# Optimization experiments

Measured on AMD Instinct MI355X. Metric: run time of the kernel, lower is better.

The kernel has to match this reference:

```python
import jax, jax.numpy as jnp
import numpy as np

B, S, D, H, DK, DV, DFF, L, V = 8, 1024, 256, 8, 32, 32, 1024, 4, 28
EPS = 1e-5
NEG = -1e9


def _ln(x, w, b):
    m = jnp.mean(x, axis=-1, keepdims=True)
    v = jnp.var(x, axis=-1, keepdims=True)
    return (x - m) * jax.lax.rsqrt(v + EPS) * w + b


def setup_inputs() -> dict:
    key = jax.random.key(0)
    ks = jax.random.split(key, 30)
    std = 0.02
    inp = {
        'input_ids': jax.random.randint(ks[0], (B, S), 0, V),
        'tok_embed': jax.random.normal(ks[1], (V, D), jnp.float32) * std,
        'pos_embed': jax.random.normal(ks[2], (S, D), jnp.float32) * std,
        'emb_ln_w': jnp.ones((D,), jnp.float32),
        'emb_ln_b': jnp.zeros((D,), jnp.float32),
        'Wq': jax.random.normal(ks[3], (L, D, H * DK), jnp.float32) * std,
        'bq': jnp.zeros((L, H * DK), jnp.float32),
        'Wk': jax.random.normal(ks[4], (L, D, H * DK), jnp.float32) * std,
        'bk': jnp.zeros((L, H * DK), jnp.float32),
        'Wv': jax.random.normal(ks[5], (L, D, H * DV), jnp.float32) * std,
        'bv': jnp.zeros((L, H * DV), jnp.float32),
        'Wo': jax.random.normal(ks[6], (L, H * DV, D), jnp.float32) * std,
        'bo': jnp.zeros((L, D), jnp.float32),
        'ln_w': jnp.ones((L, D), jnp.float32),
        'ln_b': jnp.zeros((L, D), jnp.float32),
        'W1': jax.random.normal(ks[7], (L, D, DFF), jnp.float32) * std,
        'b1': jnp.zeros((L, DFF), jnp.float32),
        'W2': jax.random.normal(ks[8], (L, DFF, D), jnp.float32) * std,
        'b2': jnp.zeros((L, D), jnp.float32),
        'ft1_w': jax.random.normal(ks[9], (D, D), jnp.float32) * std,
        'ft1_b': jnp.zeros((D,), jnp.float32),
        'ft2_w': jax.random.normal(ks[10], (D, D // 2), jnp.float32) * std,
        'ft2_b': jnp.zeros((D // 2,), jnp.float32),
        'cls_w': jax.random.normal(ks[11], (D // 2, 2), jnp.float32) * std,
        'cls_b': jnp.zeros((2,), jnp.float32),
    }
    return inp


def reference(input_ids, tok_embed, pos_embed, emb_ln_w, emb_ln_b,
              Wq, bq, Wk, bk, Wv, bv, Wo, bo, ln_w, ln_b,
              W1, b1, W2, b2, ft1_w, ft1_b, ft2_w, ft2_b, cls_w, cls_b):
    # Embedding: tok + pos, then LayerNorm
    x = tok_embed[input_ids] + pos_embed[jnp.arange(S)][None, :, :]
    x = _ln(x, emb_ln_w, emb_ln_b)
    # pad mask: True where key position is pad (token id 0); broadcast [B,1,1,S]
    pad = (input_ids == 0)[:, None, None, :]
    scale = 1.0 / np.sqrt(DK)
    for i in range(L):
        residual = x
        q = (x @ Wq[i] + bq[i]).reshape(B, S, H, DK).transpose(0, 2, 1, 3)
        k = (x @ Wk[i] + bk[i]).reshape(B, S, H, DK).transpose(0, 2, 1, 3)
        v = (x @ Wv[i] + bv[i]).reshape(B, S, H, DV).transpose(0, 2, 1, 3)
        scores = jnp.einsum('bhqd,bhkd->bhqk', q, k) * scale
        scores = jnp.where(pad, NEG, scores)
        attn = jax.nn.softmax(scores, axis=-1)
        ctx = jnp.einsum('bhqk,bhkd->bhqd', attn, v)
        ctx = ctx.transpose(0, 2, 1, 3).reshape(B, S, H * DV)
        x = _ln(ctx @ Wo[i] + bo[i] + residual, ln_w[i], ln_b[i])
        # FFN (note: original has NO residual/norm after FFN)
        x = jax.nn.relu(x @ W1[i] + b1[i]) @ W2[i] + b2[i]
    cls = x[:, 0, :]
    feat = jax.nn.relu(cls @ ft1_w + ft1_b) @ ft2_w + ft2_b  # dropout = eval no-op
    logits = feat @ cls_w + cls_b
    return logits, feat
```

## Files before the change

kernel.cpp:

```cpp
#include <hip/hip_runtime.h>
#include <math.h>

#define S_ 1024
#define D_ 256

typedef __attribute__((ext_vector_type(8))) _Float16 half8;
typedef __attribute__((ext_vector_type(4))) _Float16 half4;
typedef __attribute__((ext_vector_type(2))) _Float16 half2v;
typedef __attribute__((ext_vector_type(4))) float f32x4;
typedef __attribute__((ext_vector_type(4))) unsigned int u32x4;

__device__ __forceinline__ float wave_sum64(float x) {
    x += __shfl_xor(x, 32); x += __shfl_xor(x, 16); x += __shfl_xor(x, 8);
    x += __shfl_xor(x, 4);  x += __shfl_xor(x, 2);  x += __shfl_xor(x, 1);
    return x;
}

#define GLD16(gp, lp) __builtin_amdgcn_global_load_lds( \
    (const __attribute__((address_space(1))) void*)(gp), \
    (__attribute__((address_space(3))) void*)(lp), 16, 0, 0)

__global__ __launch_bounds__(256) void transpose_cvt(
    const float* __restrict__ src, _Float16* __restrict__ dst, int K, int N)
{
    __shared__ float tile[32][33];
    src += (size_t)blockIdx.z * K * N;
    dst += (size_t)blockIdx.z * K * N;
    const int bx = blockIdx.x * 32;
    const int by = blockIdx.y * 32;
    const int t = threadIdx.x;
    const int c = t & 31, r0 = t >> 5;
    #pragma unroll
    for (int j = 0; j < 4; ++j)
        tile[r0 + 8 * j][c] = src[(size_t)(by + r0 + 8 * j) * N + bx + c];
    __syncthreads();
    #pragma unroll
    for (int j = 0; j < 4; ++j)
        dst[(size_t)(bx + r0 + 8 * j) * K + by + c] = (_Float16)tile[c][r0 + 8 * j];
}

__global__ __launch_bounds__(256) void transpose_qkv(
    const float* __restrict__ Wq, const float* __restrict__ Wk,
    const float* __restrict__ Wv, _Float16* __restrict__ qkvT)
{
    __shared__ float tile[32][33];
    const int z = blockIdx.z, l = z / 3, m = z % 3;
    const float* src = (m == 0 ? Wq : (m == 1 ? Wk : Wv)) + (size_t)l * 65536;
    _Float16* dst = qkvT + (size_t)l * 196608 + (size_t)m * 65536;
    const int bx = blockIdx.x * 32;
    const int by = blockIdx.y * 32;
    const int t = threadIdx.x;
    const int c = t & 31, r0 = t >> 5;
    #pragma unroll
    for (int j = 0; j < 4; ++j)
        tile[r0 + 8 * j][c] = src[(size_t)(by + r0 + 8 * j) * 256 + bx + c];
    __syncthreads();
    #pragma unroll
    for (int j = 0; j < 4; ++j)
        dst[(size_t)(bx + r0 + 8 * j) * 256 + by + c] = (_Float16)tile[c][r0 + 8 * j];
}

__global__ __launch_bounds__(256) void pack_bias(
    const float* __restrict__ bq, const float* __restrict__ bk,
    const float* __restrict__ bv, float* __restrict__ bqkv)
{
    const int z = blockIdx.x, l = z / 3, m = z % 3;
    const float* s = (m == 0 ? bq : (m == 1 ? bk : bv)) + l * 256;
    bqkv[l * 768 + m * 256 + threadIdx.x] = s[threadIdx.x];
}

__global__ __launch_bounds__(256) void embed_ln_kernel(
    const int* __restrict__ ids, const float* __restrict__ tok,
    const float* __restrict__ pos, const float* __restrict__ w,
    const float* __restrict__ b, float* __restrict__ X, _Float16* __restrict__ Xh)
{
    const int wv_ = threadIdx.x >> 6, lane = threadIdx.x & 63;
    const int tokid = blockIdx.x * 4 + wv_;
    const int s = tokid & (S_ - 1);
    const int id = ids[tokid];
    float4 e = *(const float4*)&tok[id * D_ + lane * 4];
    float4 p = *(const float4*)&pos[s * D_ + lane * 4];
    float4 x = make_float4(e.x + p.x, e.y + p.y, e.z + p.z, e.w + p.w);
    float sum = x.x + x.y + x.z + x.w;
    float sq  = x.x * x.x + x.y * x.y + x.z * x.z + x.w * x.w;
    sum = wave_sum64(sum); sq = wave_sum64(sq);
    float mean = sum * (1.f / D_);
    float var  = sq * (1.f / D_) - mean * mean;
    float rs   = rsqrtf(var + 1e-5f);
    float4 wv = *(const float4*)&w[lane * 4];
    float4 bv = *(const float4*)&b[lane * 4];
    float4 o = make_float4((x.x - mean) * rs * wv.x + bv.x,
                           (x.y - mean) * rs * wv.y + bv.y,
                           (x.z - mean) * rs * wv.z + bv.z,
                           (x.w - mean) * rs * wv.w + bv.w);
    *(float4*)&X[(size_t)tokid * D_ + lane * 4] = o;
    half4 oh = { (_Float16)o.x, (_Float16)o.y, (_Float16)o.z, (_Float16)o.w };
    *(half4*)&Xh[(size_t)tokid * D_ + lane * 4] = oh;
}

__global__ __launch_bounds__(256) void ln_kernel(
    const float* __restrict__ Y, const float* __restrict__ w,
    const float* __restrict__ b, _Float16* __restrict__ Th)
{
    const int wv_ = threadIdx.x >> 6, lane = threadIdx.x & 63;
    const int tokid = blockIdx.x * 4 + wv_;
    const size_t base = (size_t)tokid * D_ + lane * 4;
    float4 x = *(const float4*)&Y[base];
    float sum = x.x + x.y + x.z + x.w;
    float sq  = x.x * x.x + x.y * x.y + x.z * x.z + x.w * x.w;
    sum = wave_sum64(sum); sq = wave_sum64(sq);
    float mean = sum * (1.f / D_);
    float var  = sq * (1.f / D_) - mean * mean;
    float rs   = rsqrtf(var + 1e-5f);
    float4 wv = *(const float4*)&w[lane * 4];
    float4 bv = *(const float4*)&b[lane * 4];
    half4 oh = { (_Float16)((x.x - mean) * rs * wv.x + bv.x),
                 (_Float16)((x.y - mean) * rs * wv.y + bv.y),
                 (_Float16)((x.z - mean) * rs * wv.z + bv.z),
                 (_Float16)((x.w - mean) * rs * wv.w + bv.w) };
    *(half4*)&Th[base] = oh;
}

template<int MODE>
__global__ __launch_bounds__(256) void gemm_f16(
    const _Float16* __restrict__ A, const _Float16* __restrict__ Bt,
    const float* __restrict__ bias, const float* __restrict__ res,
    float* __restrict__ Cf, _Float16* __restrict__ Ch,
    int K, int N)
{
    __shared__ _Float16 As[2][8192];
    const int t = threadIdx.x;
    const int wid = t >> 6, lane = t & 63;
    const int wr = wid >> 1, wc = wid & 1;
    const int m0 = blockIdx.x * 128, n0 = blockIdx.y * 64;
    const int li = lane & 15, lg = lane >> 4;
    const int srow = lane >> 3;
    const int scg = (lane & 7) ^ srow;

    f32x4 acc[4][2];
    const f32x4 zf = {0.f, 0.f, 0.f, 0.f};
    #pragma unroll
    for (int mr = 0; mr < 4; ++mr) { acc[mr][0] = zf; acc[mr][1] = zf; }

    const int KT = K >> 6;
    {
        const _Float16* Ab = A + (size_t)m0 * K;
        #pragma unroll
        for (int j = 0; j < 4; ++j) {
            int row = (wid * 4 + j) * 8 + srow;
            GLD16(Ab + (size_t)row * K + scg * 8, &As[0][(wid * 4 + j) * 512]);
        }
    }

    for (int kt = 0; kt < KT; ++kt) {
        const int cur = kt & 1;
        half8 bfr[2][2];
        #pragma unroll
        for (int nr = 0; nr < 2; ++nr) {
            const _Float16* bp = Bt + (size_t)(n0 + wc * 32 + nr * 16 + li) * K + kt * 64 + lg * 8;
            bfr[nr][0] = *(const half8*)bp;
            bfr[nr][1] = *(const half8*)(bp + 32);
        }
        if (kt + 1 < KT) {
            const _Float16* Ab = A + (size_t)m0 * K + (kt + 1) * 64;
            #pragma unroll
            for (int j = 0; j < 4; ++j) {
                int row = (wid * 4 + j) * 8 + srow;
                GLD16(Ab + (size_t)row * K + scg * 8, &As[cur ^ 1][(wid * 4 + j) * 512]);
            }
            asm volatile("s_waitcnt vmcnt(8)" ::: "memory");
        } else {
            asm volatile("s_waitcnt vmcnt(4)" ::: "memory");
        }
        __builtin_amdgcn_s_barrier();
        #pragma unroll
        for (int kk = 0; kk < 2; ++kk) {
            half8 af[4];
            #pragma unroll
            for (int mr = 0; mr < 4; ++mr) {
                int arow = wr * 64 + mr * 16 + li;
                int ablk = (kk * 4 + lg) ^ (li & 7);
                af[mr] = *(const half8*)&As[cur][arow * 64 + ablk * 8];
            }
            #pragma unroll
            for (int mr = 0; mr < 4; ++mr)
                #pragma unroll
                for (int nr = 0; nr < 2; ++nr)
                    acc[mr][nr] = __builtin_amdgcn_mfma_f32_16x16x32_f16(
                        af[mr], bfr[nr][kk], acc[mr][nr], 0, 0, 0);
        }
        __builtin_amdgcn_s_barrier();
    }

    #pragma unroll
    for (int nr = 0; nr < 2; ++nr) {
        const int n = n0 + wc * 32 + nr * 16 + li;
        const float bv = bias[n];
        #pragma unroll
        for (int mr = 0; mr < 4; ++mr) {
            #pragma unroll
            for (int r = 0; r < 4; ++r) {
                const int m = m0 + wr * 64 + mr * 16 + lg * 4 + r;
                float o = acc[mr][nr][r] + bv;
                if (MODE == 1) o = fmaxf(o, 0.f);
                if (MODE == 4) o += res[(size_t)m * N + n];
                if (MODE == 0 || MODE == 2 || MODE == 4) Cf[(size_t)m * N + n] = o;
                if (MODE == 1 || MODE == 2 || MODE == 3) Ch[(size_t)m * N + n] = (_Float16)o;
            }
        }
    }
}

__global__ __launch_bounds__(256, 4) void attn_f16_kernel(
    const _Float16* __restrict__ qkv, const int* __restrict__ ids,
    _Float16* __restrict__ ctxo)
{
    __shared__ unsigned int VTp[2][32 * 38];
    __shared__ float maskn[2][64];
    const int t = threadIdx.x;
    const int bh = blockIdx.x, b = bh >> 3, h = bh & 7;
    const int q0 = blockIdx.y * 64;
    const int wid = t >> 6;
    const int lane = t & 63;
    const int i = lane & 15;
    const int g = lane >> 4;
    const int kp = t >> 3;
    const int v0s = (t & 7) * 4;

    const size_t bS = (size_t)b * S_;
    const float scale = 0.17677669529663687f * 1.4426950408889634f;

    const half8 qf = *(const half8*)(qkv + (bS + q0 + wid * 16 + i) * 768 + h * 32 + g * 8);

    float m = -INFINITY, l = 0.f;
    f32x4 cacc[2];
    const f32x4 zf = {0.f, 0.f, 0.f, 0.f};
    cacc[0] = zf; cacc[1] = zf;

    const _Float16* kbase = qkv + 256 + (bS + i) * 768 + h * 32 + g * 8;
    const _Float16* vbase = qkv + 512 + (bS + 2 * kp) * 768 + h * 32 + v0s;

    {
        const ushort* vb = (const ushort*)vbase;
        ushort4 a0 = *(const ushort4*)vb;
        ushort4 a1 = *(const ushort4*)(vb + 768);
        VTp[0][(v0s + 0) * 38 + kp] = (unsigned)a0.x | ((unsigned)a1.x << 16);
        VTp[0][(v0s + 1) * 38 + kp] = (unsigned)a0.y | ((unsigned)a1.y << 16);
        VTp[0][(v0s + 2) * 38 + kp] = (unsigned)a0.z | ((unsigned)a1.z << 16);
        VTp[0][(v0s + 3) * 38 + kp] = (unsigned)a0.w | ((unsigned)a1.w << 16);
        if (t < 64) maskn[0][t] = (ids[bS + t] == 0) ? -1e9f : 0.f;
    }

    for (int kt = 0; kt < 16; ++kt) {
        const int cur = kt & 1;
        __syncthreads();
        ushort4 a0, a1;
        int midv = 1;
        const bool have = (kt < 15);
        if (have) {
            const ushort* vb = (const ushort*)(vbase + (size_t)(kt + 1) * 64 * 768);
            a0 = *(const ushort4*)vb;
            a1 = *(const ushort4*)(vb + 768);
            if (t < 64) midv = ids[bS + (kt + 1) * 64 + t];
        }
        const int k0 = kt * 64;
        half8 kf[4];
        const _Float16* kb = kbase + (size_t)k0 * 768;
        #pragma unroll
        for (int c = 0; c < 4; ++c) kf[c] = *(const half8*)(kb + c * 16 * 768);
        f32x4 sacc[4];
        #pragma unroll
        for (int c = 0; c < 4; ++c)
            sacc[c] = __builtin_amdgcn_mfma_f32_16x16x32_f16(kf[c], qf, zf, 0, 0, 0);
        float p[4][4];
        float tmax = -INFINITY;
        #pragma unroll
        for (int c = 0; c < 4; ++c) {
            float4 ad = *(const float4*)&maskn[cur][c * 16 + g * 4];
            p[c][0] = fmaf(sacc[c][0], scale, ad.x);
            p[c][1] = fmaf(sacc[c][1], scale, ad.y);
            p[c][2] = fmaf(sacc[c][2], scale, ad.z);
            p[c][3] = fmaf(sacc[c][3], scale, ad.w);
            tmax = fmaxf(tmax, fmaxf(fmaxf(p[c][0], p[c][1]), fmaxf(p[c][2], p[c][3])));
        }
        tmax = fmaxf(tmax, __shfl_xor(tmax, 16));
        tmax = fmaxf(tmax, __shfl_xor(tmax, 32));
        if (__any(tmax > m)) {
            float mn  = fmaxf(m, tmax);
            float fac = exp2f(m - mn);
            l *= fac;
            cacc[0] *= fac;
            cacc[1] *= fac;
            m = mn;
        }
        float psum = 0.f;
        #pragma unroll
        for (int c = 0; c < 4; ++c) {
            p[c][0] = exp2f(p[c][0] - m); p[c][1] = exp2f(p[c][1] - m);
            p[c][2] = exp2f(p[c][2] - m); p[c][3] = exp2f(p[c][3] - m);
            psum += (p[c][0] + p[c][1]) + (p[c][2] + p[c][3]);
        }
        psum += __shfl_xor(psum, 16);
        psum += __shfl_xor(psum, 32);
        l += psum;
        if (have) {
            VTp[cur ^ 1][(v0s + 0) * 38 + kp] = (unsigned)a0.x | ((unsigned)a1.x << 16);
            VTp[cur ^ 1][(v0s + 1) * 38 + kp] = (unsigned)a0.y | ((unsigned)a1.y << 16);
            VTp[cur ^ 1][(v0s + 2) * 38 + kp] = (unsigned)a0.z | ((unsigned)a1.z << 16);
            VTp[cur ^ 1][(v0s + 3) * 38 + kp] = (unsigned)a0.w | ((unsigned)a1.w << 16);
            if (t < 64) maskn[cur ^ 1][t] = (midv == 0) ? -1e9f : 0.f;
        }
        #pragma unroll
        for (int c = 0; c < 4; ++c) {
            half2v plo = __builtin_bit_cast(half2v, __builtin_amdgcn_cvt_pkrtz(p[c][0], p[c][1]));
            half2v phi = __builtin_bit_cast(half2v, __builtin_amdgcn_cvt_pkrtz(p[c][2], p[c][3]));
            half4 pb = { plo[0], plo[1], phi[0], phi[1] };
            #pragma unroll
            for (int vh = 0; vh < 2; ++vh) {
                const unsigned int* vp = &VTp[cur][(vh * 16 + i) * 38 + 8 * c + 2 * g];
                unsigned long long vv = *(const unsigned long long*)vp;
                half4 vf = __builtin_bit_cast(half4, vv);
                cacc[vh] = __builtin_amdgcn_mfma_f32_16x16x16f16(vf, pb, cacc[vh], 0, 0, 0);
            }
        }
    }
    const float inv = 1.f / l;
    _Float16* crow = ctxo + (bS + q0 + wid * 16 + i) * 256 + h * 32;
    #pragma unroll
    for (int vh = 0; vh < 2; ++vh) {
        half4 st;
        #pragma unroll
        for (int r = 0; r < 4; ++r) st[r] = (_Float16)(cacc[vh][r] * inv);
        *(half4*)&crow[vh * 16 + g * 4] = st;
    }
}

__global__ __launch_bounds__(256) void head1_kernel(
    const float* __restrict__ X, const float* __restrict__ ft1w,
    const float* __restrict__ ft1b, float* __restrict__ h1)
{
    __shared__ float clsS[8][256];
    __shared__ float ps[8][8][32];
    const int t = threadIdx.x;
    #pragma unroll
    for (int b = 0; b < 8; ++b) clsS[b][t] = X[(size_t)b * S_ * D_ + t];
    __syncthreads();
    const int n = t & 31, dg = t >> 5;
    const int gn = blockIdx.x * 32 + n;
    float s[8] = {};
    for (int dd = 0; dd < 32; ++dd) {
        int d = dg * 32 + dd;
        float w = ft1w[d * 256 + gn];
        #pragma unroll
        for (int b = 0; b < 8; ++b) s[b] = fmaf(clsS[b][d], w, s[b]);
    }
    #pragma unroll
    for (int b = 0; b < 8; ++b) ps[dg][b][n] = s[b];
    __syncthreads();
    {
        const int b = t >> 5, nn = t & 31;
        float a = 0.f;
        #pragma unroll
        for (int g = 0; g < 8; ++g) a += ps[g][b][nn];
        const int gn2 = blockIdx.x * 32 + nn;
        h1[b * 256 + gn2] = fmaxf(a + ft1b[gn2], 0.f);
    }
}

__global__ __launch_bounds__(256) void head2_kernel(
    const float* __restrict__ h1, const float* __restrict__ ft2w,
    const float* __restrict__ ft2b, float* __restrict__ featW,
    float* __restrict__ out)
{
    __shared__ float hS[8][256];
    __shared__ float ps[8][8][32];
    const int t = threadIdx.x;
    #pragma unroll
    for (int b = 0; b < 8; ++b) hS[b][t] = h1[b * 256 + t];
    __syncthreads();
    const int n = t & 31, dg = t >> 5;
    const int gn = blockIdx.x * 32 + n;
    float s[8] = {};
    for (int dd = 0; dd < 32; ++dd) {
        int d = dg * 32 + dd;
        float w = ft2w[d * 128 + gn];
        #pragma unroll
        for (int b = 0; b < 8; ++b) s[b] = fmaf(hS[b][d], w, s[b]);
    }
    #pragma unroll
    for (int b = 0; b < 8; ++b) ps[dg][b][n] = s[b];
    __syncthreads();
    {
        const int b = t >> 5, nn = t & 31;
        float a = 0.f;
        #pragma unroll
        for (int g = 0; g < 8; ++g) a += ps[g][b][nn];
        const int gn2 = blockIdx.x * 32 + nn;
        float v = a + ft2b[gn2];
        featW[b * 128 + gn2] = v;
        out[16 + b * 128 + gn2] = v;
    }
}

__global__ __launch_bounds__(64) void head3_kernel(
    const float* __restrict__ featW, const float* __restrict__ clw,
    const float* __restrict__ clb, float* __restrict__ out)
{
    const int t = threadIdx.x;
    if (t < 16) {
        const int b = t >> 1, c = t & 1;
        float s = 0.f;
        for (int d = 0; d < 128; ++d) s = fmaf(featW[b * 128 + d], clw[d * 2 + c], s);
        out[t] = s + clb[c];
    }
}

extern "C" void kernel_launch(void* const* d_in, const int* in_sizes, int n_in,
                              void* d_out, int out_size, void* d_ws, size_t ws_size,
                              hipStream_t stream)
{
    const int*   ids  = (const int*)d_in[0];
    const float* tok  = (const float*)d_in[1];
    const float* pos  = (const float*)d_in[2];
    const float* elnw = (const float*)d_in[3];
    const float* elnb = (const float*)d_in[4];
    const float* Wq   = (const float*)d_in[5];
    const float* bq   = (const float*)d_in[6];
    const float* Wk   = (const float*)d_in[7];
    const float* bk   = (const float*)d_in[8];
    const float* Wv   = (const float*)d_in[9];
    const float* bv   = (const float*)d_in[10];
    const float* Wo   = (const float*)d_in[11];
    const float* bo   = (const float*)d_in[12];
    const float* lnw  = (const float*)d_in[13];
    const float* lnb  = (const float*)d_in[14];
    const float* W1   = (const float*)d_in[15];
    const float* b1   = (const float*)d_in[16];
    const float* W2   = (const float*)d_in[17];
    const float* b2   = (const float*)d_in[18];
    const float* ft1w = (const float*)d_in[19];
    const float* ft1b = (const float*)d_in[20];
    const float* ft2w = (const float*)d_in[21];
    const float* ft2b = (const float*)d_in[22];
    const float* clw  = (const float*)d_in[23];
    const float* clb  = (const float*)d_in[24];
    float* out = (float*)d_out;

    char* ws = (char*)d_ws;
    float*    X    = (float*)(ws);
    float*    Y    = (float*)(ws + (8ull << 20));
    _Float16* Xh   = (_Float16*)(ws + (16ull << 20));
    _Float16* Th   = (_Float16*)(ws + (20ull << 20));
    _Float16* qkvb = (_Float16*)(ws + (24ull << 20));
    _Float16* ctx  = (_Float16*)(ws + (36ull << 20));
    _Float16* Hb   = (_Float16*)(ws + (24ull << 20));
    _Float16* qkvT = (_Float16*)(ws + (40ull << 20));
    _Float16* WoT  = (_Float16*)(ws + (42ull << 20));
    _Float16* W1T  = (_Float16*)(ws + (43ull << 20));
    _Float16* W2T  = (_Float16*)(ws + (45ull << 20));
    float*    bqkv = (float*)(ws + (47ull << 20));
    float*    h1W  = (float*)(ws + (47ull << 20) + (16ull << 10));
    float*    feW  = (float*)(ws + (47ull << 20) + (24ull << 10));

    transpose_qkv<<<dim3(8, 8, 12), 256, 0, stream>>>(Wq, Wk, Wv, qkvT);
    transpose_cvt<<<dim3(8, 8, 4),  256, 0, stream>>>(Wo, WoT, 256, 256);
    transpose_cvt<<<dim3(32, 8, 4), 256, 0, stream>>>(W1, W1T, 256, 1024);
    transpose_cvt<<<dim3(8, 32, 4), 256, 0, stream>>>(W2, W2T, 1024, 256);
    pack_bias<<<12, 256, 0, stream>>>(bq, bk, bv, bqkv);

    embed_ln_kernel<<<2048, 256, 0, stream>>>(ids, tok, pos, elnw, elnb, X, Xh);

    for (int i = 0; i < 4; ++i) {
        gemm_f16<3><<<dim3(64, 12), 256, 0, stream>>>(
            Xh, qkvT + (size_t)i * 196608, bqkv + i * 768, nullptr, nullptr, qkvb, 256, 768);
        attn_f16_kernel<<<dim3(64, 16), 256, 0, stream>>>(qkvb, ids, ctx);
        gemm_f16<4><<<dim3(64, 4), 256, 0, stream>>>(
            ctx, WoT + (size_t)i * 65536, bo + i * 256, X, Y, nullptr, 256, 256);
        ln_kernel<<<2048, 256, 0, stream>>>(Y, lnw + i * 256, lnb + i * 256, Th);
        gemm_f16<1><<<dim3(64, 16), 256, 0, stream>>>(
            Th, W1T + (size_t)i * 262144, b1 + i * 1024, nullptr, nullptr, Hb, 256, 1024);
        gemm_f16<2><<<dim3(64, 4), 256, 0, stream>>>(
            Hb, W2T + (size_t)i * 262144, b2 + i * 256, nullptr, X, Xh, 1024, 256);
    }

    head1_kernel<<<8, 256, 0, stream>>>(X, ft1w, ft1b, h1W);
    head2_kernel<<<4, 256, 0, stream>>>(h1W, ft2w, ft2b, feW, out);
    head3_kernel<<<1, 64, 0, stream>>>(feW, clw, clb, out);
}
```

Baseline: 447.3 us.

## Split attention KV range in two with separate combine kernel

Attention now runs as a split-K flash-decoding style pass. Each block handles half of the key/value sequence and writes unnormalized fp16 partial context plus its running max and sum. A new combine kernel merges the two halves with rescaling. The aim is to double the attention grid from 1024 to 2048 blocks and shorten the serial KV loop, at the cost of an extra launch and extra partial-result memory traffic. The partial accumulators are stored in fp16 before rescaling, which adds some precision risk.

```diff
diff --git a/kernel.cpp b/kernel.cpp
--- a/kernel.cpp
+++ b/kernel.cpp
@@ -213,13 +213,15 @@
 
 __global__ __launch_bounds__(256, 4) void attn_f16_kernel(
     const _Float16* __restrict__ qkv, const int* __restrict__ ids,
-    _Float16* __restrict__ ctxo)
+    _Float16* __restrict__ accP, float* __restrict__ mlP)
 {
     __shared__ unsigned int VTp[2][32 * 38];
     __shared__ float maskn[2][64];
     const int t = threadIdx.x;
     const int bh = blockIdx.x, b = bh >> 3, h = bh & 7;
     const int q0 = blockIdx.y * 64;
+    const int z = blockIdx.z;
+    const int kvb = z * 512;
     const int wid = t >> 6;
     const int lane = t & 63;
     const int i = lane & 15;
@@ -241,29 +243,29 @@
     const _Float16* vbase = qkv + 512 + (bS + 2 * kp) * 768 + h * 32 + v0s;
 
     {
-        const ushort* vb = (const ushort*)vbase;
+        const ushort* vb = (const ushort*)(vbase + (size_t)kvb * 768);
         ushort4 a0 = *(const ushort4*)vb;
         ushort4 a1 = *(const ushort4*)(vb + 768);
         VTp[0][(v0s + 0) * 38 + kp] = (unsigned)a0.x | ((unsigned)a1.x << 16);
         VTp[0][(v0s + 1) * 38 + kp] = (unsigned)a0.y | ((unsigned)a1.y << 16);
         VTp[0][(v0s + 2) * 38 + kp] = (unsigned)a0.z | ((unsigned)a1.z << 16);
         VTp[0][(v0s + 3) * 38 + kp] = (unsigned)a0.w | ((unsigned)a1.w << 16);
-        if (t < 64) maskn[0][t] = (ids[bS + t] == 0) ? -1e9f : 0.f;
-    }
-
-    for (int kt = 0; kt < 16; ++kt) {
+        if (t < 64) maskn[0][t] = (ids[bS + kvb + t] == 0) ? -1e9f : 0.f;
+    }
+
+    for (int kt = 0; kt < 8; ++kt) {
         const int cur = kt & 1;
         __syncthreads();
         ushort4 a0, a1;
         int midv = 1;
-        const bool have = (kt < 15);
+        const bool have = (kt < 7);
         if (have) {
-            const ushort* vb = (const ushort*)(vbase + (size_t)(kt + 1) * 64 * 768);
+            const ushort* vb = (const ushort*)(vbase + (size_t)(kvb + (kt + 1) * 64) * 768);
             a0 = *(const ushort4*)vb;
             a1 = *(const ushort4*)(vb + 768);
-            if (t < 64) midv = ids[bS + (kt + 1) * 64 + t];
-        }
-        const int k0 = kt * 64;
+            if (t < 64) midv = ids[bS + kvb + (kt + 1) * 64 + t];
+        }
+        const int k0 = kvb + kt * 64;
         half8 kf[4];
         const _Float16* kb = kbase + (size_t)k0 * 768;
         #pragma unroll
@@ -300,8 +302,6 @@
             p[c][2] = exp2f(p[c][2] - m); p[c][3] = exp2f(p[c][3] - m);
             psum += (p[c][0] + p[c][1]) + (p[c][2] + p[c][3]);
         }
-        psum += __shfl_xor(psum, 16);
-        psum += __shfl_xor(psum, 32);
         l += psum;
         if (have) {
             VTp[cur ^ 1][(v0s + 0) * 38 + kp] = (unsigned)a0.x | ((unsigned)a1.x << 16);
@@ -324,15 +324,43 @@
             }
         }
     }
-    const float inv = 1.f / l;
-    _Float16* crow = ctxo + (bS + q0 + wid * 16 + i) * 256 + h * 32;
+    l += __shfl_xor(l, 16);
+    l += __shfl_xor(l, 32);
+    const size_t rbase = (size_t)(z * 64 + bh) * 1024 + (q0 + wid * 16 + i);
     #pragma unroll
     for (int vh = 0; vh < 2; ++vh) {
         half4 st;
         #pragma unroll
-        for (int r = 0; r < 4; ++r) st[r] = (_Float16)(cacc[vh][r] * inv);
-        *(half4*)&crow[vh * 16 + g * 4] = st;
-    }
+        for (int r = 0; r < 4; ++r) st[r] = (_Float16)cacc[vh][r];
+        *(half4*)&accP[rbase * 32 + vh * 16 + g * 4] = st;
+    }
+    if (lane < 16) {
+        float2 ml; ml.x = m; ml.y = l;
+        *(float2*)&mlP[rbase * 2] = ml;
+    }
+}
+
+__global__ __launch_bounds__(256) void attn_combine_kernel(
+    const _Float16* __restrict__ accP, const float* __restrict__ mlP,
+    _Float16* __restrict__ ctxo)
+{
+    const int t = threadIdx.x;
+    const int row = blockIdx.x * 32 + (t >> 3);
+    const int v0 = (t & 7) * 4;
+    float2 ml0 = *(const float2*)&mlP[(size_t)row * 2];
+    float2 ml1 = *(const float2*)&mlP[(size_t)(65536 + row) * 2];
+    float ms = fmaxf(ml0.x, ml1.x);
+    float f0 = exp2f(ml0.x - ms), f1 = exp2f(ml1.x - ms);
+    float inv = 1.f / (ml0.y * f0 + ml1.y * f1);
+    half4 a0 = *(const half4*)&accP[(size_t)row * 32 + v0];
+    half4 a1 = *(const half4*)&accP[(size_t)(65536 + row) * 32 + v0];
+    const int bh = row >> 10, q = row & 1023;
+    const int b = bh >> 3, h = bh & 7;
+    half4 o;
+    #pragma unroll
+    for (int r = 0; r < 4; ++r)
+        o[r] = (_Float16)((f0 * (float)a0[r] + f1 * (float)a1[r]) * inv);
+    *(half4*)&ctxo[((size_t)(b * S_ + q)) * 256 + h * 32 + v0] = o;
 }
 
 __global__ __launch_bounds__(256) void head1_kernel(
@@ -461,6 +489,8 @@
     float*    bqkv = (float*)(ws + (47ull << 20));
     float*    h1W  = (float*)(ws + (47ull << 20) + (16ull << 10));
     float*    feW  = (float*)(ws + (47ull << 20) + (24ull << 10));
+    _Float16* accP = (_Float16*)(ws + (48ull << 20));
+    float*    mlP  = (float*)(ws + (57ull << 20));
 
     transpose_qkv<<<dim3(8, 8, 12), 256, 0, stream>>>(Wq, Wk, Wv, qkvT);
     transpose_cvt<<<dim3(8, 8, 4),  256, 0, stream>>>(Wo, WoT, 256, 256);
@@ -473,7 +503,8 @@
     for (int i = 0; i < 4; ++i) {
         gemm_f16<3><<<dim3(64, 12), 256, 0, stream>>>(
             Xh, qkvT + (size_t)i * 196608, bqkv + i * 768, nullptr, nullptr, qkvb, 256, 768);
-        attn_f16_kernel<<<dim3(64, 16), 256, 0, stream>>>(qkvb, ids, ctx);
+        attn_f16_kernel<<<dim3(64, 16, 2), 256, 0, stream>>>(qkvb, ids, accP, mlP);
+        attn_combine_kernel<<<2048, 256, 0, stream>>>(accP, mlP, ctx);
         gemm_f16<4><<<dim3(64, 4), 256, 0, stream>>>(
             ctx, WoT + (size_t)i * 65536, bo + i * 256, X, Y, nullptr, 256, 256);
         ln_kernel<<<2048, 256, 0, stream>>>(Y, lnw + i * 256, lnb + i * 256, Th);
```

Measured after the change: 470.0 us. 1.05x slower.

## Add 64x64-tile GEMM for N=256 layers and software-pipeline QK^T in attention

Applied to the files above, without the earlier changes.

Adds a gemm64_f16 kernel with 64x64 tiles, a double-buffered swizzled LDS A tile and B fragments read straight from global memory. It is used for the Wo and W2 projections (N=256) so the grid grows from 256 to 512 blocks and fills more CUs. In the attention kernel, the QK^T MFMA for the next key tile is issued during the current iteration, overlapping K loads and score compute with the softmax. The per-iteration cross-lane reduction of the row sum is moved to a single reduction after the loop. Costs are more B reloads from global per block and higher register pressure in attention.

```diff
diff --git a/kernel.cpp b/kernel.cpp
--- a/kernel.cpp
+++ b/kernel.cpp
@@ -211,6 +211,95 @@
     }
 }
 
+template<int MODE>
+__global__ __launch_bounds__(256) void gemm64_f16(
+    const _Float16* __restrict__ A, const _Float16* __restrict__ Bt,
+    const float* __restrict__ bias, const float* __restrict__ res,
+    float* __restrict__ Cf, _Float16* __restrict__ Ch,
+    int K, int N)
+{
+    __shared__ _Float16 As[2][4096];
+    const int t = threadIdx.x;
+    const int wid = t >> 6, lane = t & 63;
+    const int wr = wid >> 1, wc = wid & 1;
+    const int m0 = blockIdx.x * 64, n0 = blockIdx.y * 64;
+    const int li = lane & 15, lg = lane >> 4;
+    const int srow = lane >> 3;
+    const int scg = (lane & 7) ^ srow;
+
+    f32x4 acc[2][2];
+    const f32x4 zf = {0.f, 0.f, 0.f, 0.f};
+    acc[0][0] = zf; acc[0][1] = zf; acc[1][0] = zf; acc[1][1] = zf;
+
+    const int KT = K >> 6;
+    {
+        const _Float16* Ab = A + (size_t)m0 * K;
+        #pragma unroll
+        for (int j = 0; j < 2; ++j) {
+            int rb = j * 32 + wid * 8;
+            GLD16(Ab + (size_t)(rb + srow) * K + scg * 8, &As[0][rb * 64]);
+        }
+    }
+
+    for (int kt = 0; kt < KT; ++kt) {
+        const int cur = kt & 1;
+        half8 bfr[2][2];
+        #pragma unroll
+        for (int nr = 0; nr < 2; ++nr) {
+            const _Float16* bp = Bt + (size_t)(n0 + wc * 32 + nr * 16 + li) * K + kt * 64 + lg * 8;
+            bfr[nr][0] = *(const half8*)bp;
+            bfr[nr][1] = *(const half8*)(bp + 32);
+        }
+        if (kt + 1 < KT) {
+            const _Float16* Ab = A + (size_t)m0 * K + (kt + 1) * 64;
+            #pragma unroll
+            for (int j = 0; j < 2; ++j) {
+                int rb = j * 32 + wid * 8;
+                GLD16(Ab + (size_t)(rb + srow) * K + scg * 8, &As[cur ^ 1][rb * 64]);
+            }
+            asm volatile("s_waitcnt vmcnt(6)" ::: "memory");
+        } else {
+            asm volatile("s_waitcnt vmcnt(4)" ::: "memory");
+        }
+        __builtin_amdgcn_s_barrier();
+        #pragma unroll
+        for (int kk = 0; kk < 2; ++kk) {
+            half8 af[2];
+            #pragma unroll
+            for (int mr = 0; mr < 2; ++mr) {
+                int arow = wr * 32 + mr * 16 + li;
+                int ablk = (kk * 4 + lg) ^ (li & 7);
+                af[mr] = *(const half8*)&As[cur][arow * 64 + ablk * 8];
+            }
+            #pragma unroll
+            for (int mr = 0; mr < 2; ++mr)
+                #pragma unroll
+                for (int nr = 0; nr < 2; ++nr)
+                    acc[mr][nr] = __builtin_amdgcn_mfma_f32_16x16x32_f16(
+                        af[mr], bfr[nr][kk], acc[mr][nr], 0, 0, 0);
+        }
+        __builtin_amdgcn_s_barrier();
+    }
+
+    #pragma unroll
+    for (int nr = 0; nr < 2; ++nr) {
+        const int n = n0 + wc * 32 + nr * 16 + li;
+        const float bv = bias[n];
+        #pragma unroll
+        for (int mr = 0; mr < 2; ++mr) {
+            #pragma unroll
+            for (int r = 0; r < 4; ++r) {
+                const int m = m0 + wr * 32 + mr * 16 + lg * 4 + r;
+                float o = acc[mr][nr][r] + bv;
+                if (MODE == 1) o = fmaxf(o, 0.f);
+                if (MODE == 4) o += res[(size_t)m * N + n];
+                if (MODE == 0 || MODE == 2 || MODE == 4) Cf[(size_t)m * N + n] = o;
+                if (MODE == 1 || MODE == 2 || MODE == 3) Ch[(size_t)m * N + n] = (_Float16)o;
+            }
+        }
+    }
+}
+
 __global__ __launch_bounds__(256, 4) void attn_f16_kernel(
     const _Float16* __restrict__ qkv, const int* __restrict__ ids,
     _Float16* __restrict__ ctxo)
@@ -250,37 +339,37 @@
         VTp[0][(v0s + 3) * 38 + kp] = (unsigned)a0.w | ((unsigned)a1.w << 16);
         if (t < 64) maskn[0][t] = (ids[bS + t] == 0) ? -1e9f : 0.f;
     }
+    f32x4 sc[4];
+    #pragma unroll
+    for (int c = 0; c < 4; ++c)
+        sc[c] = __builtin_amdgcn_mfma_f32_16x16x32_f16(
+            *(const half8*)(kbase + c * 16 * 768), qf, zf, 0, 0, 0);
 
     for (int kt = 0; kt < 16; ++kt) {
         const int cur = kt & 1;
         __syncthreads();
         ushort4 a0, a1;
         int midv = 1;
+        half8 kf[4];
         const bool have = (kt < 15);
         if (have) {
             const ushort* vb = (const ushort*)(vbase + (size_t)(kt + 1) * 64 * 768);
             a0 = *(const ushort4*)vb;
             a1 = *(const ushort4*)(vb + 768);
             if (t < 64) midv = ids[bS + (kt + 1) * 64 + t];
-        }
-        const int k0 = kt * 64;
-        half8 kf[4];
-        const _Float16* kb = kbase + (size_t)k0 * 768;
-        #pragma unroll
-        for (int c = 0; c < 4; ++c) kf[c] = *(const half8*)(kb + c * 16 * 768);
-        f32x4 sacc[4];
-        #pragma unroll
-        for (int c = 0; c < 4; ++c)
-            sacc[c] = __builtin_amdgcn_mfma_f32_16x16x32_f16(kf[c], qf, zf, 0, 0, 0);
+            const _Float16* kb = kbase + (size_t)(kt + 1) * 64 * 768;
+            #pragma unroll
+            for (int c = 0; c < 4; ++c) kf[c] = *(const half8*)(kb + c * 16 * 768);
+        }
         float p[4][4];
         float tmax = -INFINITY;
         #pragma unroll
         for (int c = 0; c < 4; ++c) {
             float4 ad = *(const float4*)&maskn[cur][c * 16 + g * 4];
-            p[c][0] = fmaf(sacc[c][0], scale, ad.x);
-            p[c][1] = fmaf(sacc[c][1], scale, ad.y);
-            p[c][2] = fmaf(sacc[c][2], scale, ad.z);
-            p[c][3] = fmaf(sacc[c][3], scale, ad.w);
+            p[c][0] = fmaf(sc[c][0], scale, ad.x);
+            p[c][1] = fmaf(sc[c][1], scale, ad.y);
+            p[c][2] = fmaf(sc[c][2], scale, ad.z);
+            p[c][3] = fmaf(sc[c][3], scale, ad.w);
             tmax = fmaxf(tmax, fmaxf(fmaxf(p[c][0], p[c][1]), fmaxf(p[c][2], p[c][3])));
         }
         tmax = fmaxf(tmax, __shfl_xor(tmax, 16));
@@ -300,9 +389,12 @@
             p[c][2] = exp2f(p[c][2] - m); p[c][3] = exp2f(p[c][3] - m);
             psum += (p[c][0] + p[c][1]) + (p[c][2] + p[c][3]);
         }
-        psum += __shfl_xor(psum, 16);
-        psum += __shfl_xor(psum, 32);
         l += psum;
+        if (have) {
+            #pragma unroll
+            for (int c = 0; c < 4; ++c)
+                sc[c] = __builtin_amdgcn_mfma_f32_16x16x32_f16(kf[c], qf, zf, 0, 0, 0);
+        }
         if (have) {
             VTp[cur ^ 1][(v0s + 0) * 38 + kp] = (unsigned)a0.x | ((unsigned)a1.x << 16);
             VTp[cur ^ 1][(v0s + 1) * 38 + kp] = (unsigned)a0.y | ((unsigned)a1.y << 16);
@@ -324,6 +416,8 @@
             }
         }
     }
+    l += __shfl_xor(l, 16);
+    l += __shfl_xor(l, 32);
     const float inv = 1.f / l;
     _Float16* crow = ctxo + (bS + q0 + wid * 16 + i) * 256 + h * 32;
     #pragma unroll
@@ -474,12 +568,12 @@
         gemm_f16<3><<<dim3(64, 12), 256, 0, stream>>>(
             Xh, qkvT + (size_t)i * 196608, bqkv + i * 768, nullptr, nullptr, qkvb, 256, 768);
         attn_f16_kernel<<<dim3(64, 16), 256, 0, stream>>>(qkvb, ids, ctx);
-        gemm_f16<4><<<dim3(64, 4), 256, 0, stream>>>(
+        gemm64_f16<4><<<dim3(128, 4), 256, 0, stream>>>(
             ctx, WoT + (size_t)i * 65536, bo + i * 256, X, Y, nullptr, 256, 256);
         ln_kernel<<<2048, 256, 0, stream>>>(Y, lnw + i * 256, lnb + i * 256, Th);
         gemm_f16<1><<<dim3(64, 16), 256, 0, stream>>>(
             Th, W1T + (size_t)i * 262144, b1 + i * 1024, nullptr, nullptr, Hb, 256, 1024);
-        gemm_f16<2><<<dim3(64, 4), 256, 0, stream>>>(
+        gemm64_f16<2><<<dim3(128, 4), 256, 0, stream>>>(
             Hb, W2T + (size_t)i * 262144, b2 + i * 256, nullptr, X, Xh, 1024, 256);
     }
 
```

New measurement: 430.9 us. 3.7% less time.
